# Optimization experiments

Hardware: AMD Instinct MI355X
Metric: run time of the kernel (lower is better)

## Reference

```python
import jax, jax.numpy as jnp
import numpy as np

N, E, HN, K = 4096, 8192, 1024, 8
NF, EF = 128, 64
NH = [256, 256]
EH = [64, 64]
EMB = NH[-1] + len(EH)  # 258
BN_EPS = 1e-5


def setup_inputs() -> dict:
    key = jax.random.key(0)
    ks = jax.random.split(key, 16)

    def nrm(k, shape, fan):
        return jax.random.normal(k, shape, jnp.float32) / np.float32(np.sqrt(fan))

    return {
        "X_n": jax.random.normal(ks[0], (N, NF), jnp.float32),
        "X_e": jax.random.normal(ks[1], (E, EF), jnp.float32),
        # row-normalized-ish adjacency and scaled Laplacian to keep activations bounded
        "A_tilde": jax.random.uniform(ks[2], (N, N), jnp.float32) / np.float32(N),
        "L1_tilde": jax.random.normal(ks[3], (E, E), jnp.float32) / np.float32(np.sqrt(E)),
        "B1": jax.random.normal(ks[4], (N, E), jnp.float32) / np.float32(np.sqrt(E)),
        # GNN params (Linear stores weight as [out, in])
        "gnn_W1": nrm(ks[5], (NH[0], NF), NF), "gnn_b1": jnp.zeros((NH[0],), jnp.float32),
        "gnn_W2": nrm(ks[6], (NH[1], NH[0]), NH[0]), "gnn_b2": jnp.zeros((NH[1],), jnp.float32),
        # HoSC layer 1: in=EF, out=EH[0]
        "hosc_W1": nrm(ks[7], (EH[0], EF), EF), "hosc_b1": jnp.zeros((EH[0],), jnp.float32),
        "bn1_g": jnp.ones((EH[0],), jnp.float32), "bn1_b": jnp.zeros((EH[0],), jnp.float32),
        # HoSC layer 2: in=1 (after channel-max), out=EH[1]
        "hosc_W2": nrm(ks[8], (EH[1], 1), 1), "hosc_b2": jnp.zeros((EH[1],), jnp.float32),
        "bn2_g": jnp.ones((EH[1],), jnp.float32), "bn2_b": jnp.zeros((EH[1],), jnp.float32),
        # heads
        "node_W": nrm(ks[9], (1, EMB), EMB), "node_b": jnp.zeros((1,), jnp.float32),
        "edge_W": nrm(ks[10], (1, len(EH)), len(EH)), "edge_b": jnp.zeros((1,), jnp.float32),
        "hyper_W": nrm(ks[11], (1, EMB), EMB), "hyper_b": jnp.zeros((1,), jnp.float32),
        "hyperedges": jax.random.randint(ks[12], (HN, K), 0, N, jnp.int64),
    }


def _bn(x, g, b):
    # training-mode BatchNorm1d: biased batch statistics over rows
    m = jnp.mean(x, axis=0)
    v = jnp.var(x, axis=0)
    return g * (x - m) / jnp.sqrt(v + BN_EPS) + b


def _hosc_layer(Z, L1, W, bias, g, b):
    Zt = Z @ W.T + bias            # [E, out]
    Zc = L1 @ Zt                   # [E, out]
    Zp = jax.nn.relu(_bn(Zc, g, b))
    return jnp.max(Zp, axis=1, keepdims=True)  # [E, 1]


def reference(X_n, X_e, A_tilde, L1_tilde, B1,
              gnn_W1, gnn_b1, gnn_W2, gnn_b2,
              hosc_W1, hosc_b1, bn1_g, bn1_b,
              hosc_W2, hosc_b2, bn2_g, bn2_b,
              node_W, node_b, edge_W, edge_b, hyper_W, hyper_b,
              hyperedges):
    # --- GNN over nodes ---
    H = jax.nn.relu((A_tilde @ X_n) @ gnn_W1.T + gnn_b1)   # [N, 256]
    H_n = jax.nn.relu((A_tilde @ H) @ gnn_W2.T + gnn_b2)   # [N, 256]

    # --- HoSC over edges ---
    Z1 = _hosc_layer(X_e, L1_tilde, hosc_W1, hosc_b1, bn1_g, bn1_b)  # [E, 1]
    Z2 = _hosc_layer(Z1, L1_tilde, hosc_W2, hosc_b2, bn2_g, bn2_b)   # [E, 1]
    Z_H = jnp.concatenate([Z1, Z2], axis=1)                 # [E, 2]

    # --- fuse edge info into nodes ---
    H_e = B1 @ Z_H                                          # [N, 2]
    Hcat = jnp.concatenate([H_n, H_e], axis=1)              # [N, 258]

    node_prob = jax.nn.sigmoid(Hcat @ node_W.T + node_b).squeeze(-1)  # [N]
    edge_prob = jax.nn.sigmoid(Z_H @ edge_W.T + edge_b).squeeze(-1)   # [E]

    # vectorized hyperedge gather-mean-linear-sigmoid (fixed-size hyperedges)
    hfeat = Hcat[hyperedges].mean(axis=1)                   # [HN, 258]
    hyperedge_prob = jax.nn.sigmoid(hfeat @ hyper_W.T + hyper_b)  # [HN, 1]

    return node_prob, edge_prob, hyperedge_prob, Hcat
```

## Files before the change

kernel.cpp:

```cpp
#include <hip/hip_runtime.h>
#include <hip/hip_bf16.h>

using f32x4  = __attribute__((ext_vector_type(4))) float;
using u32x4  = __attribute__((ext_vector_type(4))) unsigned int;
using bf16x8 = __attribute__((ext_vector_type(8))) short;

__device__ __forceinline__ ushort f2bf(float x) {
    union { __hip_bfloat16 h; ushort u; } cv;
    cv.h = __float2bfloat16(x);
    return cv.u;
}
__device__ __forceinline__ unsigned pk2(float lo, float hi) {
    return (unsigned)f2bf(lo) | ((unsigned)f2bf(hi) << 16);
}
__device__ __forceinline__ float sigmoidf_(float x) { return 1.f / (1.f + expf(-x)); }

template<int NSUM, bool A_BF16, bool SPLIT, bool RELU, bool BF16_OUT, bool HAS_BIAS>
__global__ __launch_bounds__(256)
void gemm_kernel(const void* __restrict__ Avoid, const ushort* __restrict__ B,
                 const float* __restrict__ bias, float* __restrict__ Cf,
                 ushort* __restrict__ Cb, int M, int N, int K, int ldc,
                 int kPerChunk, long pStride)
{
    __shared__ ushort As[128 * 40];
    __shared__ ushort Bs[64 * 40];
    const int tid  = threadIdx.x;
    const int lane = tid & 63;
    const int wid  = tid >> 6;
    const int wr   = wid >> 1, wc = wid & 1;
    const int g    = lane >> 4, lr = lane & 15;
    const long m0  = (long)blockIdx.x * 128;
    const int  n0  = blockIdx.y * 64;

    int kbeg = 0, kend = K;
    if (SPLIT) { kbeg = blockIdx.z * kPerChunk; kend = kbeg + kPerChunk; if (kend > K) kend = K; }

    const int bkr = tid & 31;
    const int bcb = tid >> 5;

    const float*  Af = (const float*)Avoid;
    const ushort* Ab = (const ushort*)Avoid;

    f32x4 pa[4];
    u32x4 pab[2];
    u32x4 pb;

    auto loadT = [&](int k0) {
        if (A_BF16) {
#pragma unroll
            for (int i = 0; i < 2; i++) {
                int s = tid + 256 * i; int row = s >> 2, c8 = s & 3;
                pab[i] = *(const u32x4*)(Ab + (m0 + row) * (long)K + k0 + c8 * 8);
            }
        } else {
#pragma unroll
            for (int i = 0; i < 4; i++) {
                int s = tid + 256 * i; int row = s >> 3, c4 = s & 7;
                const float* base = Af + (m0 + row) * (long)K + k0 + c4 * 4;
                f32x4 v = *(const f32x4*)base;
                if (NSUM > 0) {
#pragma unroll
                    for (int z = 1; z < NSUM; z++) v += *(const f32x4*)(base + z * pStride);
                }
                pa[i] = v;
            }
        }
        pb = *(const u32x4*)(B + (long)(k0 + bkr) * N + n0 + bcb * 8);
    };
    auto storeT = [&]() {
        if (A_BF16) {
#pragma unroll
            for (int i = 0; i < 2; i++) {
                int s = tid + 256 * i; int row = s >> 2, c8 = s & 3;
                *(u32x4*)(&As[row * 40 + c8 * 8]) = pab[i];
            }
        } else {
#pragma unroll
            for (int i = 0; i < 4; i++) {
                int s = tid + 256 * i; int row = s >> 3, c4 = s & 7;
                ushort4 w;
                w.x = f2bf(pa[i].x); w.y = f2bf(pa[i].y);
                w.z = f2bf(pa[i].z); w.w = f2bf(pa[i].w);
                *(ushort4*)(&As[row * 40 + c4 * 4]) = w;
            }
        }
        const ushort* p8 = (const ushort*)&pb;
#pragma unroll
        for (int j = 0; j < 8; j++) Bs[(bcb * 8 + j) * 40 + bkr] = p8[j];
    };

    f32x4 acc[4][2] = {};

    const int nk = (kend - kbeg) >> 5;
    loadT(kbeg);
    for (int t = 0; t < nk; ++t) {
        storeT();
        __syncthreads();
        if (t + 1 < nk) loadT(kbeg + ((t + 1) << 5));
        bf16x8 af[4], bfr[2];
#pragma unroll
        for (int fm = 0; fm < 4; fm++)
            af[fm] = *(const bf16x8*)(&As[(wr * 64 + fm * 16 + lr) * 40 + g * 8]);
#pragma unroll
        for (int fn = 0; fn < 2; fn++)
            bfr[fn] = *(const bf16x8*)(&Bs[(wc * 32 + fn * 16 + lr) * 40 + g * 8]);
#pragma unroll
        for (int fm = 0; fm < 4; fm++)
#pragma unroll
            for (int fn = 0; fn < 2; fn++)
                acc[fm][fn] = __builtin_amdgcn_mfma_f32_16x16x32_bf16(af[fm], bfr[fn], acc[fm][fn], 0, 0, 0);
        __syncthreads();
    }

    if (SPLIT) {
        float* P = Cf + (long)blockIdx.z * M * N;
#pragma unroll
        for (int fm = 0; fm < 4; fm++)
#pragma unroll
            for (int fn = 0; fn < 2; fn++)
#pragma unroll
                for (int rr = 0; rr < 4; rr++) {
                    long row = m0 + wr * 64 + fm * 16 + g * 4 + rr;
                    int  col = n0 + wc * 32 + fn * 16 + lr;
                    P[row * N + col] = acc[fm][fn][rr];
                }
    } else {
#pragma unroll
        for (int fm = 0; fm < 4; fm++)
#pragma unroll
            for (int fn = 0; fn < 2; fn++)
#pragma unroll
                for (int rr = 0; rr < 4; rr++) {
                    long row = m0 + wr * 64 + fm * 16 + g * 4 + rr;
                    int  col = n0 + wc * 32 + fn * 16 + lr;
                    float v = acc[fm][fn][rr];
                    if (HAS_BIAS) v += bias[col];
                    if (RELU) v = fmaxf(v, 0.f);
                    if (BF16_OUT) Cb[row * ldc + col] = f2bf(v);
                    else          Cf[row * ldc + col] = v;
                }
    }
}

__global__ __launch_bounds__(256) void prep_k(const float* __restrict__ A, ushort* __restrict__ Abf,
                                              const float* __restrict__ Xn, ushort* __restrict__ Xnb,
                                              const float* __restrict__ W1, ushort* __restrict__ W1t,
                                              const float* __restrict__ W2, ushort* __restrict__ W2t,
                                              const float* __restrict__ Xe, const float* __restrict__ Wh,
                                              const float* __restrict__ hb, ushort* __restrict__ Zt1,
                                              float* __restrict__ stats)
{
    int b = blockIdx.x, t = threadIdx.x;
    if (b < 8192) {
        long j = (long)b * 256 + t;
        f32x4 v0 = ((const f32x4*)A)[2 * j];
        f32x4 v1 = ((const f32x4*)A)[2 * j + 1];
        u32x4 w;
        w.x = pk2(v0.x, v0.y); w.y = pk2(v0.z, v0.w);
        w.z = pk2(v1.x, v1.y); w.w = pk2(v1.z, v1.w);
        ((u32x4*)Abf)[j] = w;
    } else if (b < 8448) {
        long j = (long)(b - 8192) * 256 + t;
        f32x4 v0 = ((const f32x4*)Xn)[2 * j];
        f32x4 v1 = ((const f32x4*)Xn)[2 * j + 1];
        u32x4 w;
        w.x = pk2(v0.x, v0.y); w.y = pk2(v0.z, v0.w);
        w.z = pk2(v1.x, v1.y); w.w = pk2(v1.z, v1.w);
        ((u32x4*)Xnb)[j] = w;
    } else if (b < 8576) {
        int j = (b - 8448) * 256 + t;
        int i = j >> 8, o = j & 255;
        W1t[j] = f2bf(W1[o * 128 + i]);
    } else if (b < 8832) {
        int j = (b - 8576) * 256 + t;
        int i = j >> 8, o = j & 255;
        W2t[j] = f2bf(W2[o * 256 + i]);
    } else if (b < 10880) {
        int row = (b - 8832) * 4 + (t >> 6);
        int o   = t & 63;
        const float* xr = Xe + (long)row * 64;
        const float* wr = Wh + (long)o * 64;
        float acc = hb[o];
#pragma unroll 8
        for (int i = 0; i < 64; i++) acc += xr[i] * wr[i];
        Zt1[(long)row * 64 + o] = f2bf(acc);
    } else {
        if (t < 192) stats[t] = 0.f;
    }
}

__global__ __launch_bounds__(256) void bnred_k(const float* __restrict__ P,
                                               float* __restrict__ Zc,
                                               float* __restrict__ gsum, float* __restrict__ gsq)
{
    const long MN = 8192 * 64;
    int b = blockIdx.x, t = threadIdx.x;
    int c = t & 63, rg = t >> 6;
    float sx = 0.f, sq = 0.f;
    int base = b * 32 + rg;
#pragma unroll 4
    for (int i = 0; i < 8; i++) {
        long idx = (long)(base + 4 * i) * 64 + c;
        float x = 0.f;
#pragma unroll
        for (int z = 0; z < 8; z++) x += P[idx + z * MN];
        Zc[idx] = x;
        sx += x; sq += x * x;
    }
    __shared__ float ls[256], lq[256];
    ls[t] = sx; lq[t] = sq;
    __syncthreads();
    if (t < 64) {
        float a = ls[t] + ls[t + 64] + ls[t + 128] + ls[t + 192];
        float q = lq[t] + lq[t + 64] + lq[t + 128] + lq[t + 192];
        atomicAdd(&gsum[t], a);
        atomicAdd(&gsq[t], q);
    }
}

__global__ __launch_bounds__(256) void z1_k(const float* __restrict__ Zc,
                                            const float* __restrict__ gsum, const float* __restrict__ gsq,
                                            const float* __restrict__ g, const float* __restrict__ b,
                                            float* __restrict__ Z1)
{
    int w = threadIdx.x >> 6, lane = threadIdx.x & 63;
    int row = blockIdx.x * 4 + w;
    const float inv = 1.f / 8192.f;
    float m = gsum[lane] * inv;
    float v = gsq[lane] * inv - m * m;
    float x = Zc[row * 64 + lane];
    float y = fmaxf(g[lane] * (x - m) * rsqrtf(v + 1e-5f) + b[lane], 0.f);
#pragma unroll
    for (int o = 32; o > 0; o >>= 1) y = fmaxf(y, __shfl_xor(y, o));
    if (lane == 0) Z1[row] = y;
}

__global__ __launch_bounds__(256) void pass2_k(const float* __restrict__ L1, const float* __restrict__ Z1,
                                               float* __restrict__ s, float* __restrict__ r)
{
    int row = blockIdx.x, t = threadIdx.x;
    int l = t & 63, w = t >> 6;
    const f32x4* rp = (const f32x4*)(L1 + (long)row * 8192);
    const f32x4* z4 = (const f32x4*)Z1;
    float as = 0.f, ar = 0.f;
#pragma unroll 4
    for (int k = 0; k < 8; k++) {
        f32x4 v = rp[t + 256 * k];
        f32x4 z = z4[t + 256 * k];
        as += v.x * z.x + v.y * z.y + v.z * z.z + v.w * z.w;
        ar += v.x + v.y + v.z + v.w;
    }
#pragma unroll
    for (int o = 32; o > 0; o >>= 1) { as += __shfl_xor(as, o); ar += __shfl_xor(ar, o); }
    __shared__ float sw[4], rw[4];
    if (l == 0) { sw[w] = as; rw[w] = ar; }
    __syncthreads();
    if (t == 0) {
        s[row] = sw[0] + sw[1] + sw[2] + sw[3];
        r[row] = rw[0] + rw[1] + rw[2] + rw[3];
    }
}

__global__ __launch_bounds__(1024) void stats2_k(const float* __restrict__ s, const float* __restrict__ r,
                                                 float* __restrict__ S5)
{
    int t = threadIdx.x, l = t & 63, w = t >> 6;
    float Ss = 0, Sr = 0, Sss = 0, Srr = 0, Ssr = 0;
    for (int i = t; i < 8192; i += 1024) {
        float sv = s[i], rv = r[i];
        Ss += sv; Sr += rv; Sss += sv * sv; Srr += rv * rv; Ssr += sv * rv;
    }
#pragma unroll
    for (int o = 32; o > 0; o >>= 1) {
        Ss += __shfl_xor(Ss, o); Sr += __shfl_xor(Sr, o);
        Sss += __shfl_xor(Sss, o); Srr += __shfl_xor(Srr, o); Ssr += __shfl_xor(Ssr, o);
    }
    __shared__ float buf[16][5];
    if (l == 0) { buf[w][0] = Ss; buf[w][1] = Sr; buf[w][2] = Sss; buf[w][3] = Srr; buf[w][4] = Ssr; }
    __syncthreads();
    if (t < 5) {
        float a = 0.f;
#pragma unroll
        for (int i = 0; i < 16; i++) a += buf[i][t];
        S5[t] = a;
    }
}

__global__ __launch_bounds__(256) void z2_edge_k(const float* __restrict__ s, const float* __restrict__ r,
                                                 const float* __restrict__ S,
                                                 const float* __restrict__ W2, const float* __restrict__ b2,
                                                 const float* __restrict__ g2, const float* __restrict__ bb2,
                                                 const float* __restrict__ eW, const float* __restrict__ eb,
                                                 const float* __restrict__ Z1,
                                                 float* __restrict__ Z2, float* __restrict__ edge_out)
{
    int w = threadIdx.x >> 6, lane = threadIdx.x & 63;
    int row = blockIdx.x * 4 + w;
    const float inv = 1.f / 8192.f;
    float ms = S[0] * inv, mr = S[1] * inv;
    float vs = S[2] * inv - ms * ms;
    float vr = S[3] * inv - mr * mr;
    float cv = S[4] * inv - ms * mr;
    float w2 = W2[lane], bz = b2[lane];
    float mc = w2 * ms + bz * mr;
    float vc = w2 * w2 * vs + 2.f * w2 * bz * cv + bz * bz * vr;
    float x  = w2 * s[row] + bz * r[row];
    float y  = fmaxf(g2[lane] * (x - mc) * rsqrtf(vc + 1e-5f) + bb2[lane], 0.f);
#pragma unroll
    for (int o = 32; o > 0; o >>= 1) y = fmaxf(y, __shfl_xor(y, o));
    if (lane == 0) {
        Z2[row] = y;
        float e = Z1[row] * eW[0] + y * eW[1] + eb[0];
        edge_out[row] = sigmoidf_(e);
    }
}

__global__ __launch_bounds__(256) void he_node_k(const float* __restrict__ B1, const float* __restrict__ Z1,
                                                 const float* __restrict__ Z2, float* __restrict__ hcat,
                                                 const float* __restrict__ nW, const float* __restrict__ nb,
                                                 float* __restrict__ node_out)
{
    int n = blockIdx.x, t = threadIdx.x;
    int l = t & 63, w = t >> 6;
    const f32x4* rp  = (const f32x4*)(B1 + (long)n * 8192);
    const f32x4* z1v = (const f32x4*)Z1;
    const f32x4* z2v = (const f32x4*)Z2;
    float a1 = 0.f, a2 = 0.f;
#pragma unroll 4
    for (int k = 0; k < 8; k++) {
        f32x4 v = rp[t + 256 * k];
        f32x4 p = z1v[t + 256 * k];
        f32x4 q = z2v[t + 256 * k];
        a1 += v.x * p.x + v.y * p.y + v.z * p.z + v.w * p.w;
        a2 += v.x * q.x + v.y * q.y + v.z * q.z + v.w * q.w;
    }
    float d = hcat[(long)n * 258 + t] * nW[t];
#pragma unroll
    for (int o = 32; o > 0; o >>= 1) {
        a1 += __shfl_xor(a1, o); a2 += __shfl_xor(a2, o); d += __shfl_xor(d, o);
    }
    __shared__ float s1[4], s2[4], s3[4];
    if (l == 0) { s1[w] = a1; s2[w] = a2; s3[w] = d; }
    __syncthreads();
    if (t == 0) {
        float A1 = s1[0] + s1[1] + s1[2] + s1[3];
        float A2 = s2[0] + s2[1] + s2[2] + s2[3];
        float D  = s3[0] + s3[1] + s3[2] + s3[3];
        hcat[(long)n * 258 + 256] = A1;
        hcat[(long)n * 258 + 257] = A2;
        node_out[n] = sigmoidf_(D + A1 * nW[256] + A2 * nW[257] + nb[0]);
    }
}

__global__ __launch_bounds__(256) void hyper_k(const void* __restrict__ he_idx,
                                               const float* __restrict__ hcat,
                                               const float* __restrict__ hW, const float* __restrict__ hb,
                                               float* __restrict__ out)
{
    int w = threadIdx.x >> 6, lane = threadIdx.x & 63;
    int h = blockIdx.x * 4 + w;
    const unsigned int* u = (const unsigned int*)he_idx;
    unsigned int odd = u[2 * lane + 1];
    bool is64 = __all(odd == 0u);
    float acc = 0.f;
    for (int k = 0; k < 8; k++) {
        int idx;
        if (is64) idx = (int)((const long long*)he_idx)[h * 8 + k];
        else      idx = ((const int*)he_idx)[h * 8 + k];
        const float* hr = hcat + (long)idx * 258;
        for (int d = lane; d < 258; d += 64) acc += hr[d] * hW[d];
    }
    acc *= 0.125f;
#pragma unroll
    for (int o = 32; o > 0; o >>= 1) acc += __shfl_xor(acc, o);
    if (lane == 0) out[h] = sigmoidf_(acc + hb[0]);
}

extern "C" void kernel_launch(void* const* d_in, const int* in_sizes, int n_in,
                              void* d_out, int out_size, void* d_ws, size_t ws_size,
                              hipStream_t stream)
{
    const float* X_n  = (const float*)d_in[0];
    const float* X_e  = (const float*)d_in[1];
    const float* A_t  = (const float*)d_in[2];
    const float* L1   = (const float*)d_in[3];
    const float* B1   = (const float*)d_in[4];
    const float* gW1  = (const float*)d_in[5];
    const float* gb1  = (const float*)d_in[6];
    const float* gW2  = (const float*)d_in[7];
    const float* gb2  = (const float*)d_in[8];
    const float* hW1  = (const float*)d_in[9];
    const float* hb1  = (const float*)d_in[10];
    const float* bn1g = (const float*)d_in[11];
    const float* bn1b = (const float*)d_in[12];
    const float* hW2  = (const float*)d_in[13];
    const float* hb2  = (const float*)d_in[14];
    const float* bn2g = (const float*)d_in[15];
    const float* bn2b = (const float*)d_in[16];
    const float* nW   = (const float*)d_in[17];
    const float* nb   = (const float*)d_in[18];
    const float* eW   = (const float*)d_in[19];
    const float* ebb  = (const float*)d_in[20];
    const float* yW   = (const float*)d_in[21];
    const float* yb   = (const float*)d_in[22];
    const void*  he   = d_in[23];

    float* out       = (float*)d_out;
    float* out_node  = out;
    float* out_edge  = out + 4096;
    float* out_hyper = out + 12288;
    float* hcat      = out + 13312;

    size_t off = 0;
    auto alloc = [&](size_t bytes) {
        void* p = (char*)d_ws + off;
        off = (off + bytes + 255) & ~(size_t)255;
        return p;
    };
    ushort* Abf   = (ushort*)alloc((size_t)4096 * 4096 * 2);
    ushort* Xn_bf = (ushort*)alloc(4096 * 128 * 2);
    ushort* W1t   = (ushort*)alloc(128 * 256 * 2);
    ushort* W2t   = (ushort*)alloc(256 * 256 * 2);
    ushort* Zt1   = (ushort*)alloc(8192 * 64 * 2);
    float*  Zc1   = (float*)alloc(8192 * 64 * 4);
    float*  stats = (float*)alloc(256 * 4);
    float*  gsum  = stats;
    float*  gsq   = stats + 64;
    float*  S5    = stats + 128;
    float*  Z1    = (float*)alloc(8192 * 4);
    float*  Z2    = (float*)alloc(8192 * 4);
    float*  sbuf  = (float*)alloc(8192 * 4);
    float*  rbuf  = (float*)alloc(8192 * 4);
    float*  P     = (float*)alloc((size_t)8192 * 64 * 8 * 4);

    prep_k<<<10881, 256, 0, stream>>>(A_t, Abf, X_n, Xn_bf, gW1, W1t, gW2, W2t,
                                      X_e, hW1, hb1, Zt1, stats);

    gemm_kernel<0, true, true, false, false, false><<<dim3(32, 2, 4), 256, 0, stream>>>(
        Abf, Xn_bf, nullptr, P, nullptr, 4096, 128, 4096, 128, 1024, 0);
    gemm_kernel<4, false, false, true, true, true><<<dim3(32, 4, 1), 256, 0, stream>>>(
        P, W1t, gb1, nullptr, (ushort*)Zc1 , 4096, 256, 128, 256, 0,
        (long)4096 * 128);
    ushort* H_bf = (ushort*)Zc1;
    gemm_kernel<0, true, true, false, false, false><<<dim3(32, 4, 2), 256, 0, stream>>>(
        Abf, H_bf, nullptr, P, nullptr, 4096, 256, 4096, 256, 2048, 0);
    gemm_kernel<2, false, false, true, false, true><<<dim3(32, 4, 1), 256, 0, stream>>>(
        P, W2t, gb2, hcat, nullptr, 4096, 256, 256, 258, 0, (long)4096 * 256);

    gemm_kernel<0, false, true, false, false, false><<<dim3(64, 1, 8), 256, 0, stream>>>(
        L1, Zt1, nullptr, P, nullptr, 8192, 64, 8192, 64, 1024, 0);
    bnred_k<<<256, 256, 0, stream>>>(P, Zc1, gsum, gsq);
    z1_k<<<2048, 256, 0, stream>>>(Zc1, gsum, gsq, bn1g, bn1b, Z1);
    pass2_k<<<8192, 256, 0, stream>>>(L1, Z1, sbuf, rbuf);
    stats2_k<<<1, 1024, 0, stream>>>(sbuf, rbuf, S5);
    z2_edge_k<<<2048, 256, 0, stream>>>(sbuf, rbuf, S5, hW2, hb2, bn2g, bn2b,
                                        eW, ebb, Z1, Z2, out_edge);
    he_node_k<<<4096, 256, 0, stream>>>(B1, Z1, Z2, hcat, nW, nb, out_node);
    hyper_k<<<256, 256, 0, stream>>>(he, hcat, yW, yb, out_hyper);
}
```

Measured before the change: 303.8 us.

## Reassociate GNN matmuls and co-launch independent GNN/HoSC stages in merged kernels

Computes (A@X)@W1 as A@(X@W1) by projecting X_n through W1 in the prep kernel, and does the same for the second GNN layer, so bias+ReLU gets applied while loading the A operand of the next projection GEMM. Independent GNN and HoSC stages (L1 GEMM with A GEMM, bnred with W2 GEMM, A GEMM with z1, hcat reduction with pass2) are merged into dual-role kernels to cut launches and fill the GPU with co-scheduled work. The trade-off is that the big A GEMMs now have N=256 instead of 128 for layer one, which adds FLOPs, and the fp32 row projection in prep is a naive loop.

```diff
diff --git a/kernel.cpp b/kernel.cpp
--- a/kernel.cpp
+++ b/kernel.cpp
@@ -15,25 +15,25 @@
 }
 __device__ __forceinline__ float sigmoidf_(float x) { return 1.f / (1.f + expf(-x)); }
 
-template<int NSUM, bool A_BF16, bool SPLIT, bool RELU, bool BF16_OUT, bool HAS_BIAS>
-__global__ __launch_bounds__(256)
-void gemm_kernel(const void* __restrict__ Avoid, const ushort* __restrict__ B,
-                 const float* __restrict__ bias, float* __restrict__ Cf,
-                 ushort* __restrict__ Cb, int M, int N, int K, int ldc,
-                 int kPerChunk, long pStride)
-{
-    __shared__ ushort As[128 * 40];
-    __shared__ ushort Bs[64 * 40];
+template<int NSUM, bool A_BF16, bool ABR, bool SPLIT, bool RELU, bool BF16_OUT, bool HAS_BIAS>
+__device__ __forceinline__ void gemm_body(
+    ushort* As, ushort* Bs,
+    const void* __restrict__ Avoid, const ushort* __restrict__ B,
+    const float* __restrict__ abias, const float* __restrict__ bias,
+    float* __restrict__ Cf, ushort* __restrict__ Cb,
+    int M, int N, int K, int ldc, int kPerChunk, long pStride,
+    int bx, int by, int bz)
+{
     const int tid  = threadIdx.x;
     const int lane = tid & 63;
     const int wid  = tid >> 6;
     const int wr   = wid >> 1, wc = wid & 1;
     const int g    = lane >> 4, lr = lane & 15;
-    const long m0  = (long)blockIdx.x * 128;
-    const int  n0  = blockIdx.y * 64;
+    const long m0  = (long)bx * 128;
+    const int  n0  = by * 64;
 
     int kbeg = 0, kend = K;
-    if (SPLIT) { kbeg = blockIdx.z * kPerChunk; kend = kbeg + kPerChunk; if (kend > K) kend = K; }
+    if (SPLIT) { kbeg = bz * kPerChunk; kend = kbeg + kPerChunk; if (kend > K) kend = K; }
 
     const int bkr = tid & 31;
     const int bcb = tid >> 5;
@@ -61,6 +61,13 @@
                 if (NSUM > 0) {
 #pragma unroll
                     for (int z = 1; z < NSUM; z++) v += *(const f32x4*)(base + z * pStride);
+                }
+                if (ABR) {
+                    f32x4 bq = *(const f32x4*)(abias + k0 + c4 * 4);
+                    v.x = fmaxf(v.x + bq.x, 0.f);
+                    v.y = fmaxf(v.y + bq.y, 0.f);
+                    v.z = fmaxf(v.z + bq.z, 0.f);
+                    v.w = fmaxf(v.w + bq.w, 0.f);
                 }
                 pa[i] = v;
             }
@@ -113,7 +120,7 @@
     }
 
     if (SPLIT) {
-        float* P = Cf + (long)blockIdx.z * M * N;
+        float* P = Cf + (long)bz * M * N;
 #pragma unroll
         for (int fm = 0; fm < 4; fm++)
 #pragma unroll
@@ -142,14 +149,15 @@
     }
 }
 
-__global__ __launch_bounds__(256) void prep_k(const float* __restrict__ A, ushort* __restrict__ Abf,
-                                              const float* __restrict__ Xn, ushort* __restrict__ Xnb,
-                                              const float* __restrict__ W1, ushort* __restrict__ W1t,
-                                              const float* __restrict__ W2, ushort* __restrict__ W2t,
-                                              const float* __restrict__ Xe, const float* __restrict__ Wh,
-                                              const float* __restrict__ hb, ushort* __restrict__ Zt1,
-                                              float* __restrict__ stats)
-{
+__global__ __launch_bounds__(256)
+void prep_k(const float* __restrict__ A, ushort* __restrict__ Abf,
+            const float* __restrict__ Xn, const float* __restrict__ W1, ushort* __restrict__ T1,
+            const float* __restrict__ Xe, const float* __restrict__ Wh,
+            const float* __restrict__ hb, ushort* __restrict__ Zt1,
+            const float* __restrict__ W2, ushort* __restrict__ W2t,
+            float* __restrict__ stats)
+{
+    __shared__ float xs[1024];
     int b = blockIdx.x, t = threadIdx.x;
     if (b < 8192) {
         long j = (long)b * 256 + t;
@@ -159,24 +167,21 @@
         w.x = pk2(v0.x, v0.y); w.y = pk2(v0.z, v0.w);
         w.z = pk2(v1.x, v1.y); w.w = pk2(v1.z, v1.w);
         ((u32x4*)Abf)[j] = w;
-    } else if (b < 8448) {
-        long j = (long)(b - 8192) * 256 + t;
-        f32x4 v0 = ((const f32x4*)Xn)[2 * j];
-        f32x4 v1 = ((const f32x4*)Xn)[2 * j + 1];
-        u32x4 w;
-        w.x = pk2(v0.x, v0.y); w.y = pk2(v0.z, v0.w);
-        w.z = pk2(v1.x, v1.y); w.w = pk2(v1.z, v1.w);
-        ((u32x4*)Xnb)[j] = w;
-    } else if (b < 8576) {
-        int j = (b - 8448) * 256 + t;
-        int i = j >> 8, o = j & 255;
-        W1t[j] = f2bf(W1[o * 128 + i]);
-    } else if (b < 8832) {
-        int j = (b - 8576) * 256 + t;
-        int i = j >> 8, o = j & 255;
-        W2t[j] = f2bf(W2[o * 256 + i]);
-    } else if (b < 10880) {
-        int row = (b - 8832) * 4 + (t >> 6);
+    } else if (b < 8704) {
+        int r0 = (b - 8192) * 8;
+        for (int idx = t; idx < 1024; idx += 256) xs[idx] = Xn[(long)r0 * 128 + idx];
+        __syncthreads();
+        float acc[8] = {};
+        const float* wrow = W1 + (long)t * 128;
+        for (int i = 0; i < 128; i++) {
+            float w = wrow[i];
+#pragma unroll
+            for (int r = 0; r < 8; r++) acc[r] += xs[r * 128 + i] * w;
+        }
+#pragma unroll
+        for (int r = 0; r < 8; r++) T1[(long)(r0 + r) * 256 + t] = f2bf(acc[r]);
+    } else if (b < 10752) {
+        int row = (b - 8704) * 4 + (t >> 6);
         int o   = t & 63;
         const float* xr = Xe + (long)row * 64;
         const float* wr = Wh + (long)o * 64;
@@ -184,17 +189,21 @@
 #pragma unroll 8
         for (int i = 0; i < 64; i++) acc += xr[i] * wr[i];
         Zt1[(long)row * 64 + o] = f2bf(acc);
+    } else if (b < 11008) {
+        int j = (b - 10752) * 256 + t;
+        int i = j >> 8, o = j & 255;
+        W2t[j] = f2bf(W2[o * 256 + i]);
     } else {
-        if (t < 192) stats[t] = 0.f;
-    }
-}
-
-__global__ __launch_bounds__(256) void bnred_k(const float* __restrict__ P,
-                                               float* __restrict__ Zc,
-                                               float* __restrict__ gsum, float* __restrict__ gsq)
+        if (t < 256) stats[t] = 0.f;
+    }
+}
+
+__device__ __forceinline__ void bnred_body(int b, const float* __restrict__ P,
+                                           float* __restrict__ Zc,
+                                           float* __restrict__ gsum, float* __restrict__ gsq)
 {
     const long MN = 8192 * 64;
-    int b = blockIdx.x, t = threadIdx.x;
+    int t = threadIdx.x;
     int c = t & 63, rg = t >> 6;
     float sx = 0.f, sq = 0.f;
     int base = b * 32 + rg;
@@ -218,27 +227,28 @@
     }
 }
 
-__global__ __launch_bounds__(256) void z1_k(const float* __restrict__ Zc,
-                                            const float* __restrict__ gsum, const float* __restrict__ gsq,
-                                            const float* __restrict__ g, const float* __restrict__ b,
-                                            float* __restrict__ Z1)
+__device__ __forceinline__ void z1_body(int b, const float* __restrict__ Zc,
+                                        const float* __restrict__ gsum, const float* __restrict__ gsq,
+                                        const float* __restrict__ g, const float* __restrict__ bb,
+                                        float* __restrict__ Z1)
 {
     int w = threadIdx.x >> 6, lane = threadIdx.x & 63;
-    int row = blockIdx.x * 4 + w;
+    int row = b * 4 + w;
     const float inv = 1.f / 8192.f;
     float m = gsum[lane] * inv;
     float v = gsq[lane] * inv - m * m;
     float x = Zc[row * 64 + lane];
-    float y = fmaxf(g[lane] * (x - m) * rsqrtf(v + 1e-5f) + b[lane], 0.f);
+    float y = fmaxf(g[lane] * (x - m) * rsqrtf(v + 1e-5f) + bb[lane], 0.f);
 #pragma unroll
     for (int o = 32; o > 0; o >>= 1) y = fmaxf(y, __shfl_xor(y, o));
     if (lane == 0) Z1[row] = y;
 }
 
-__global__ __launch_bounds__(256) void pass2_k(const float* __restrict__ L1, const float* __restrict__ Z1,
-                                               float* __restrict__ s, float* __restrict__ r)
-{
-    int row = blockIdx.x, t = threadIdx.x;
+__device__ __forceinline__ void pass2_body(int row, const float* __restrict__ L1,
+                                           const float* __restrict__ Z1,
+                                           float* __restrict__ s, float* __restrict__ r)
+{
+    int t = threadIdx.x;
     int l = t & 63, w = t >> 6;
     const f32x4* rp = (const f32x4*)(L1 + (long)row * 8192);
     const f32x4* z4 = (const f32x4*)Z1;
@@ -259,6 +269,87 @@
         s[row] = sw[0] + sw[1] + sw[2] + sw[3];
         r[row] = rw[0] + rw[1] + rw[2] + rw[3];
     }
+}
+
+__device__ __forceinline__ void hcatred_body(int b, const float* __restrict__ P2,
+                                             const float* __restrict__ b2, float* __restrict__ hcat)
+{
+    const long MNq = (long)4096 * 256 / 4;
+    int j = b * 256 + threadIdx.x;
+    int row = j >> 6, c4 = (j & 63) * 4;
+    const f32x4* Q = (const f32x4*)P2;
+    f32x4 v = Q[j] + Q[j + MNq] + Q[j + 2 * MNq] + Q[j + 3 * MNq];
+    f32x4 bq = *(const f32x4*)(b2 + c4);
+    float* dst = hcat + (long)row * 258 + c4;
+    float2 lo = { fmaxf(v.x + bq.x, 0.f), fmaxf(v.y + bq.y, 0.f) };
+    float2 hi = { fmaxf(v.z + bq.z, 0.f), fmaxf(v.w + bq.w, 0.f) };
+    *(float2*)dst = lo;
+    *(float2*)(dst + 2) = hi;
+}
+
+__global__ __launch_bounds__(256)
+void dual_a_k(const float* __restrict__ L1, const ushort* __restrict__ Zt1, float* __restrict__ Pa,
+              const ushort* __restrict__ Abf, const ushort* __restrict__ T1, float* __restrict__ Pb)
+{
+    __shared__ ushort As[128 * 40];
+    __shared__ ushort Bs[64 * 40];
+    int bid = blockIdx.x;
+    if (bid < 512) {
+        gemm_body<0, false, false, true, false, false, false>(
+            As, Bs, L1, Zt1, nullptr, nullptr, Pa, nullptr,
+            8192, 64, 8192, 64, 1024, 0, bid & 63, 0, bid >> 6);
+    } else {
+        int b = bid - 512;
+        gemm_body<0, true, false, true, false, false, false>(
+            As, Bs, Abf, T1, nullptr, nullptr, Pb, nullptr,
+            4096, 256, 4096, 256, 1024, 0, b & 31, (b >> 5) & 3, b >> 7);
+    }
+}
+
+__global__ __launch_bounds__(256)
+void dual_b_k(const float* __restrict__ Pb, const float* __restrict__ gb1,
+              const ushort* __restrict__ W2t, ushort* __restrict__ T2,
+              const float* __restrict__ Pa, float* __restrict__ Zc1,
+              float* __restrict__ gsum, float* __restrict__ gsq)
+{
+    __shared__ ushort As[128 * 40];
+    __shared__ ushort Bs[64 * 40];
+    int bid = blockIdx.x;
+    if (bid < 128) {
+        gemm_body<4, false, true, false, false, true, false>(
+            As, Bs, Pb, W2t, gb1, nullptr, nullptr, T2,
+            4096, 256, 256, 256, 0, (long)4096 * 256, bid & 31, bid >> 5, 0);
+    } else {
+        bnred_body(bid - 128, Pa, Zc1, gsum, gsq);
+    }
+}
+
+__global__ __launch_bounds__(256)
+void dual_c_k(const ushort* __restrict__ Abf, const ushort* __restrict__ T2, float* __restrict__ Pa,
+              const float* __restrict__ Zc1, const float* __restrict__ gsum,
+              const float* __restrict__ gsq, const float* __restrict__ bn1g,
+              const float* __restrict__ bn1b, float* __restrict__ Z1)
+{
+    __shared__ ushort As[128 * 40];
+    __shared__ ushort Bs[64 * 40];
+    int bid = blockIdx.x;
+    if (bid < 512) {
+        gemm_body<0, true, false, true, false, false, false>(
+            As, Bs, Abf, T2, nullptr, nullptr, Pa, nullptr,
+            4096, 256, 4096, 256, 1024, 0, bid & 31, (bid >> 5) & 3, bid >> 7);
+    } else {
+        z1_body(bid - 512, Zc1, gsum, gsq, bn1g, bn1b, Z1);
+    }
+}
+
+__global__ __launch_bounds__(256)
+void dual_d_k(const float* __restrict__ Pa, const float* __restrict__ gb2, float* __restrict__ hcat,
+              const float* __restrict__ L1, const float* __restrict__ Z1,
+              float* __restrict__ s, float* __restrict__ r)
+{
+    int bid = blockIdx.x;
+    if (bid < 1024) hcatred_body(bid, Pa, gb2, hcat);
+    else            pass2_body(bid - 1024, L1, Z1, s, r);
 }
 
 __global__ __launch_bounds__(1024) void stats2_k(const float* __restrict__ s, const float* __restrict__ r,
@@ -418,10 +509,10 @@
         return p;
     };
     ushort* Abf   = (ushort*)alloc((size_t)4096 * 4096 * 2);
-    ushort* Xn_bf = (ushort*)alloc(4096 * 128 * 2);
-    ushort* W1t   = (ushort*)alloc(128 * 256 * 2);
+    ushort* T1    = (ushort*)alloc(4096 * 256 * 2);
+    ushort* T2    = (ushort*)alloc(4096 * 256 * 2);
+    ushort* Zt1   = (ushort*)alloc(8192 * 64 * 2);
     ushort* W2t   = (ushort*)alloc(256 * 256 * 2);
-    ushort* Zt1   = (ushort*)alloc(8192 * 64 * 2);
     float*  Zc1   = (float*)alloc(8192 * 64 * 4);
     float*  stats = (float*)alloc(256 * 4);
     float*  gsum  = stats;
@@ -431,30 +522,26 @@
     float*  Z2    = (float*)alloc(8192 * 4);
     float*  sbuf  = (float*)alloc(8192 * 4);
     float*  rbuf  = (float*)alloc(8192 * 4);
-    float*  P     = (float*)alloc((size_t)8192 * 64 * 8 * 4);
-
-    prep_k<<<10881, 256, 0, stream>>>(A_t, Abf, X_n, Xn_bf, gW1, W1t, gW2, W2t,
-                                      X_e, hW1, hb1, Zt1, stats);
-
-    gemm_kernel<0, true, true, false, false, false><<<dim3(32, 2, 4), 256, 0, stream>>>(
-        Abf, Xn_bf, nullptr, P, nullptr, 4096, 128, 4096, 128, 1024, 0);
-    gemm_kernel<4, false, false, true, true, true><<<dim3(32, 4, 1), 256, 0, stream>>>(
-        P, W1t, gb1, nullptr, (ushort*)Zc1 , 4096, 256, 128, 256, 0,
-        (long)4096 * 128);
-    ushort* H_bf = (ushort*)Zc1;
-    gemm_kernel<0, true, true, false, false, false><<<dim3(32, 4, 2), 256, 0, stream>>>(
-        Abf, H_bf, nullptr, P, nullptr, 4096, 256, 4096, 256, 2048, 0);
-    gemm_kernel<2, false, false, true, false, true><<<dim3(32, 4, 1), 256, 0, stream>>>(
-        P, W2t, gb2, hcat, nullptr, 4096, 256, 256, 258, 0, (long)4096 * 256);
-
-    gemm_kernel<0, false, true, false, false, false><<<dim3(64, 1, 8), 256, 0, stream>>>(
-        L1, Zt1, nullptr, P, nullptr, 8192, 64, 8192, 64, 1024, 0);
-    bnred_k<<<256, 256, 0, stream>>>(P, Zc1, gsum, gsq);
-    z1_k<<<2048, 256, 0, stream>>>(Zc1, gsum, gsq, bn1g, bn1b, Z1);
-    pass2_k<<<8192, 256, 0, stream>>>(L1, Z1, sbuf, rbuf);
+    float*  Pa    = (float*)alloc((size_t)8192 * 64 * 8 * 4);
+    float*  Pb    = (float*)alloc((size_t)4096 * 256 * 4 * 4);
+
+    prep_k<<<11009, 256, 0, stream>>>(A_t, Abf, X_n, gW1, T1, X_e, hW1, hb1, Zt1,
+                                      gW2, W2t, stats);
+
+    dual_a_k<<<1024, 256, 0, stream>>>(L1, Zt1, Pa, Abf, T1, Pb);
+
+    dual_b_k<<<384, 256, 0, stream>>>(Pb, gb1, W2t, T2, Pa, Zc1, gsum, gsq);
+
+    dual_c_k<<<2560, 256, 0, stream>>>(Abf, T2, Pa, Zc1, gsum, gsq, bn1g, bn1b, Z1);
+
+    dual_d_k<<<9216, 256, 0, stream>>>(Pa, gb2, hcat, L1, Z1, sbuf, rbuf);
+
     stats2_k<<<1, 1024, 0, stream>>>(sbuf, rbuf, S5);
+
     z2_edge_k<<<2048, 256, 0, stream>>>(sbuf, rbuf, S5, hW2, hb2, bn2g, bn2b,
                                         eW, ebb, Z1, Z2, out_edge);
+
     he_node_k<<<4096, 256, 0, stream>>>(B1, Z1, Z2, hcat, nW, nb, out_node);
+
     hyper_k<<<256, 256, 0, stream>>>(he, hcat, yW, yb, out_hyper);
 }
```

After: 291.6 us. -4.0%, faster.
